# Kernel optimization log

Measured on AMD Instinct MI355X. Metric: run time of the kernel, lower is better.

The kernel has to match this reference:

```python
import jax, jax.numpy as jnp
import numpy as np

B, CATT, D, H, W = 4, 8, 48, 128, 256
CF, EMB, HEADS, WIN = 80, 64, 4, 3
WIN2 = WIN * WIN
HEAD_DIM = EMB // HEADS
SCALE = HEAD_DIM ** -0.5


def setup_inputs() -> dict:
    key = jax.random.key(0)
    ks = jax.random.split(key, 7)
    attn_vol = jax.random.normal(ks[0], (B, CATT, D, H, W), dtype=jnp.float32)
    feat_map = jax.random.normal(ks[1], (B, CF, H, W), dtype=jnp.float32)
    # disp_gap in [0,4) so roughly half the pixels satisfy (disp_gap >= 2)
    disp_gap = jax.random.uniform(ks[2], (B, 1, H, W), dtype=jnp.float32) * 4.0
    xav = (6.0 / (EMB + CF)) ** 0.5
    Wq = jax.random.uniform(ks[3], (EMB, CF), jnp.float32, -xav, xav)
    Wk = jax.random.uniform(ks[4], (EMB, CF), jnp.float32, -xav, xav)
    Wv = jax.random.uniform(ks[5], (EMB, CF), jnp.float32, -xav, xav)
    # out_proj weight is zero-initialized in the module; use small random for a
    # non-degenerate correctness baseline
    Wo = jax.random.normal(ks[6], (CATT, EMB), dtype=jnp.float32) * 0.02
    return {"attn_vol": attn_vol, "feat_map": feat_map, "disp_gap": disp_gap,
            "Wq": Wq, "Wk": Wk, "Wv": Wv, "Wo": Wo}


def _unfold3x3_torch_layout(x):
    # x: (B, E, H, W) -> (B, N, WIN2, E) matching torch's
    # unfold(...).transpose(1,2).view(B, N, win2, emb), where unfold channel
    # index is c*9 + w (channel-major). The subsequent view therefore MIXES
    # channels and window positions; we reproduce that exactly.
    b, e, h, w = x.shape
    p = WIN // 2
    xp = jnp.pad(x, ((0, 0), (0, 0), (p, p), (p, p)))
    pat = jnp.stack([xp[:, :, i:i + h, j:j + w]
                     for i in range(WIN) for j in range(WIN)], axis=2)  # (B,E,9,H,W)
    pat = pat.reshape(b, e * WIN2, h * w)          # torch unfold layout c*9+w
    pat = pat.transpose(0, 2, 1)                   # (B, N, E*9)
    return pat.reshape(b, h * w, WIN2, e)          # faithful (mixed) view


def reference(attn_vol, feat_map, disp_gap, Wq, Wk, Wv, Wo):
    b, c_att, d, h, w = attn_vol.shape
    n = h * w
    Q = jnp.einsum('bchw,ec->behw', feat_map, Wq)
    K = jnp.einsum('bchw,ec->behw', feat_map, Wk)
    V = jnp.einsum('bchw,ec->behw', feat_map, Wv)

    Ku = _unfold3x3_torch_layout(K)  # (B, N, 9, EMB)
    Vu = _unfold3x3_torch_layout(V)

    # split heads
    Qh = Q.reshape(b, EMB, n).transpose(0, 2, 1)
    Qh = Qh.reshape(b, n, HEADS, HEAD_DIM).transpose(0, 2, 1, 3)          # (B,h,N,hd)
    Kh = Ku.reshape(b, n, WIN2, HEADS, HEAD_DIM).transpose(0, 3, 1, 2, 4)  # (B,h,N,9,hd)
    Vh = Vu.reshape(b, n, WIN2, HEADS, HEAD_DIM).transpose(0, 3, 1, 2, 4)

    scores = jnp.einsum('bhnd,bhnwd->bhnw', Qh, Kh) * SCALE
    probs = jax.nn.softmax(scores, axis=-1)
    ctx = jnp.einsum('bhnw,bhnwd->bhnd', probs, Vh)                        # (B,h,N,hd)

    ctx = ctx.transpose(0, 2, 1, 3).reshape(b, n, EMB)
    delta2d = ctx.transpose(0, 2, 1).reshape(b, EMB, h, w)
    delta2d = jnp.einsum('behw,ae->bahw', delta2d, Wo)                     # (B,CATT,H,W)

    mask = (disp_gap >= 2.0).reshape(b, 1, 1, h, w)
    delta = jnp.where(mask, 0.0, delta2d[:, :, None, :, :])               # (B,CATT,D,H,W)
    return attn_vol + delta
```

## Files before the change

kernel.cpp:

```cpp
#include <hip/hip_runtime.h>
#include <math.h>

namespace {
constexpr int Bc   = 4;
constexpr int CATT = 8;
constexpr int Hh   = 128;
constexpr int Ww   = 256;
constexpr int CF   = 80;
constexpr int EMB  = 64;
constexpr int Nn   = Hh * Ww;
constexpr float SCALE = 0.25f;

constexpr int ROWP  = 264;
constexpr int PLANE = 130 * ROWP;
constexpr size_t WS_KVQ   = 0;
constexpr size_t WS_DELTA = (size_t)Bc * 192 * PLANE;
constexpr size_t WS_WT    = WS_DELTA + (size_t)Bc * CATT * Nn;
constexpr size_t WS_WOT   = WS_WT + (size_t)CF * 192;
constexpr size_t WS_END   = WS_WOT + 512;
constexpr size_t NEED_BYTES = WS_END * 4;

constexpr size_t OWS_KV    = 0;
constexpr size_t OWS_DELTA = (size_t)Bc * Nn * 128;
constexpr size_t OWS_WTKV  = OWS_DELTA + (size_t)Bc * CATT * Nn;
constexpr size_t OWS_WTQ   = OWS_WTKV + (size_t)CF * 128;
}


__global__ void prep_new_k(const float* __restrict__ Wq,
                           const float* __restrict__ Wk,
                           const float* __restrict__ Wv,
                           const float* __restrict__ Wo,
                           float* __restrict__ wt,
                           float* __restrict__ wot,
                           float* __restrict__ kvq) {
  const int t = blockIdx.x * blockDim.x + threadIdx.x;
  const int stride = gridDim.x * blockDim.x;
  for (int i = t; i < CF * 192; i += stride) {
    const int c = i / 192, o = i % 192;
    float v;
    if (o < 64)       v = Wq[o * CF + c] * SCALE;
    else if (o < 128) v = Wk[(o - 64) * CF + c];
    else              v = Wv[(o - 128) * CF + c];
    wt[i] = v;
  }
  for (int i = t; i < 512; i += stride) {
    const int e = i >> 3, a = i & 7;
    wot[i] = Wo[a * EMB + e];
  }
  const int HALO = 1552;
  for (int i = t; i < Bc * 192 * HALO; i += stride) {
    const int plane = i / HALO;
    const int r = i % HALO;
    int row, col;
    if (r < 264)        { row = 0;   col = r; }
    else if (r < 528)   { row = 129; col = r - 264; }
    else {
      const int rr = r - 528;
      row = (rr >> 3) + 1;
      const int c8 = rr & 7;
      col = (c8 < 4) ? c8 : (260 + c8 - 4);
    }
    kvq[(size_t)plane * PLANE + row * ROWP + col] = 0.f;
  }
}

__global__ __launch_bounds__(256) void qkv_new_k(const float* __restrict__ feat,
                                                 const float* __restrict__ wt,
                                                 float* __restrict__ kvq) {
  __shared__ float lf[CF][64];
  const int b  = blockIdx.y;
  const int n0 = blockIdx.x * 64;
  const int t  = threadIdx.x;

  const float* fb = feat + (size_t)b * CF * Nn + n0;
  for (int i = t; i < CF * 64; i += 256) {
    const int c = i >> 6, p = i & 63;
    lf[c][p] = fb[(size_t)c * Nn + p];
  }
  __syncthreads();

  const int og = t >> 4;
  const int p4 = (t & 15) * 4;

  float acc[12][4];
#pragma unroll
  for (int o = 0; o < 12; ++o)
#pragma unroll
    for (int j = 0; j < 4; ++j) acc[o][j] = 0.f;

  for (int c = 0; c < CF; ++c) {
    const float4 fv = *(const float4*)&lf[c][p4];
    const float fa[4] = {fv.x, fv.y, fv.z, fv.w};
    const float4 w0 = *(const float4*)&wt[c * 192 + og * 12];
    const float4 w1 = *(const float4*)&wt[c * 192 + og * 12 + 4];
    const float4 w2 = *(const float4*)&wt[c * 192 + og * 12 + 8];
    const float wv12[12] = {w0.x, w0.y, w0.z, w0.w, w1.x, w1.y, w1.z, w1.w,
                            w2.x, w2.y, w2.z, w2.w};
#pragma unroll
    for (int o = 0; o < 12; ++o)
#pragma unroll
      for (int j = 0; j < 4; ++j) acc[o][j] = fmaf(wv12[o], fa[j], acc[o][j]);
  }

  const int h = n0 >> 8, w0c = n0 & 255;
  float* bbase = kvq + (size_t)b * 192 * PLANE;
  const int rowoff = (h + 1) * ROWP + (w0c + 4) + p4;
#pragma unroll
  for (int o = 0; o < 12; ++o) {
    const int oo = og * 12 + o;
    *(float4*)&bbase[(size_t)oo * PLANE + rowoff] =
        make_float4(acc[o][0], acc[o][1], acc[o][2], acc[o][3]);
  }
}

template <int HD>
__device__ __forceinline__ void attn_core(const float* __restrict__ kb, int coff,
                                          const float* __restrict__ lwot,
                                          float* __restrict__ part) {
  float q16[16];
#pragma unroll
  for (int i = 0; i < 16; ++i)
    q16[i] = kb[(size_t)(HD * 16 + i) * PLANE + coff];

  float sc[9];
#pragma unroll
  for (int w2 = 0; w2 < 9; ++w2) {
    float s = 0.f;
#pragma unroll
    for (int i = 0; i < 16; ++i) {
      const int f = w2 * 64 + HD * 16 + i;
      const int e = f / 9, widx = f % 9;
      const int D = (widx / 3 - 1) * ROWP + (widx % 3 - 1);
      s = fmaf(q16[i], kb[(size_t)(64 + e) * PLANE + coff + D], s);
    }
    sc[w2] = s;
  }

  float m = sc[0];
#pragma unroll
  for (int w2 = 1; w2 < 9; ++w2) m = fmaxf(m, sc[w2]);
  float probs[9], ssum = 0.f;
#pragma unroll
  for (int w2 = 0; w2 < 9; ++w2) {
    probs[w2] = __expf(sc[w2] - m);
    ssum += probs[w2];
  }
  const float inv = 1.f / ssum;
#pragma unroll
  for (int w2 = 0; w2 < 9; ++w2) probs[w2] *= inv;

  float ctx[16];
#pragma unroll
  for (int i = 0; i < 16; ++i) {
    float c = 0.f;
#pragma unroll
    for (int w2 = 0; w2 < 9; ++w2) {
      const int f = w2 * 64 + HD * 16 + i;
      const int e = f / 9, widx = f % 9;
      const int D = (widx / 3 - 1) * ROWP + (widx % 3 - 1);
      c = fmaf(probs[w2], kb[(size_t)(128 + e) * PLANE + coff + D], c);
    }
    ctx[i] = c;
  }

#pragma unroll
  for (int a = 0; a < 8; ++a) {
    float p = 0.f;
#pragma unroll
    for (int i = 0; i < 16; ++i)
      p = fmaf(lwot[(HD * 16 + i) * 8 + a], ctx[i], p);
    part[a] = p;
  }
}

__global__ __launch_bounds__(256) void attn_new_k(const float* __restrict__ kvq,
                                                  const float* __restrict__ wot,
                                                  const float* __restrict__ disp,
                                                  float* __restrict__ delta) {
  __shared__ float lwot[512];
  __shared__ float lpart[4 * 576];
  const int b = blockIdx.y;
  const int t = threadIdx.x;
  for (int i = t; i < 512; i += 256) lwot[i] = wot[i];
  __syncthreads();

  const int hd = t >> 6, lane = t & 63;
  const int n = blockIdx.x * 64 + lane;
  const int h = n >> 8, w = n & 255;
  const int coff = (h + 1) * ROWP + (w + 4);
  const float* kb = kvq + (size_t)b * 192 * PLANE;

  float part[8];
  switch (hd) {
    case 0: attn_core<0>(kb, coff, lwot, part); break;
    case 1: attn_core<1>(kb, coff, lwot, part); break;
    case 2: attn_core<2>(kb, coff, lwot, part); break;
    default: attn_core<3>(kb, coff, lwot, part); break;
  }
#pragma unroll
  for (int a = 0; a < 8; ++a) lpart[hd * 576 + lane * 9 + a] = part[a];
  __syncthreads();

  const int px = t & 63, ag = t >> 6;
  const int nn = blockIdx.x * 64 + px;
  const bool zero = disp[(size_t)b * Nn + nn] >= 2.0f;
  float* dout = delta + (size_t)b * CATT * Nn + nn;
#pragma unroll
  for (int k = 0; k < 2; ++k) {
    const int a = ag * 2 + k;
    const float s = lpart[0 * 576 + px * 9 + a] + lpart[1 * 576 + px * 9 + a] +
                    lpart[2 * 576 + px * 9 + a] + lpart[3 * 576 + px * 9 + a];
    dout[(size_t)a * Nn] = zero ? 0.f : s;
  }
}

__global__ void prep_weights_k(const float* __restrict__ Wq,
                               const float* __restrict__ Wk,
                               const float* __restrict__ Wv,
                               float* __restrict__ wtkv,
                               float* __restrict__ wtq) {
  const int t = blockIdx.x * blockDim.x + threadIdx.x;
  const int stride = gridDim.x * blockDim.x;
  for (int i = t; i < CF * 128; i += stride) {
    const int c = i >> 7, o = i & 127;
    wtkv[i] = (o < 64) ? Wk[o * CF + c] : Wv[(o - 64) * CF + c];
  }
  for (int i = t; i < CF * 64; i += stride) {
    const int c = i >> 6, e = i & 63;
    wtq[i] = Wq[e * CF + c] * SCALE;
  }
}

__global__ __launch_bounds__(256) void qkv_k(const float* __restrict__ feat,
                                             const float* __restrict__ wtkv,
                                             float* __restrict__ kv) {
  __shared__ float lf[CF][64];
  const int b  = blockIdx.y;
  const int n0 = blockIdx.x * 64;
  const int t  = threadIdx.x;
  const float* fb = feat + (size_t)b * CF * Nn + n0;
  for (int i = t; i < CF * 64; i += 256) {
    const int c = i >> 6, p = i & 63;
    lf[c][p] = fb[(size_t)c * Nn + p];
  }
  __syncthreads();
  const int og = t >> 4;
  const int p4 = (t & 15) * 4;
  float acc[8][4];
#pragma unroll
  for (int o = 0; o < 8; ++o)
#pragma unroll
    for (int j = 0; j < 4; ++j) acc[o][j] = 0.f;
  for (int c = 0; c < CF; ++c) {
    const float4 fv = *(const float4*)&lf[c][p4];
    const float fa[4] = {fv.x, fv.y, fv.z, fv.w};
    const float4 wa = *(const float4*)&wtkv[c * 128 + og * 8];
    const float4 wb = *(const float4*)&wtkv[c * 128 + og * 8 + 4];
    const float wv8[8] = {wa.x, wa.y, wa.z, wa.w, wb.x, wb.y, wb.z, wb.w};
#pragma unroll
    for (int o = 0; o < 8; ++o)
#pragma unroll
      for (int j = 0; j < 4; ++j) acc[o][j] = fmaf(wv8[o], fa[j], acc[o][j]);
  }
  float* outb = kv + ((size_t)b * Nn + n0) * 128;
#pragma unroll
  for (int j = 0; j < 4; ++j) {
    const int p = p4 + j;
    *(float4*)&outb[(size_t)p * 128 + og * 8] =
        make_float4(acc[0][j], acc[1][j], acc[2][j], acc[3][j]);
    *(float4*)&outb[(size_t)p * 128 + og * 8 + 4] =
        make_float4(acc[4][j], acc[5][j], acc[6][j], acc[7][j]);
  }
}

__global__ __launch_bounds__(256) void attn_k(const float* __restrict__ feat,
                                              const float* __restrict__ kvbuf,
                                              const float* __restrict__ wtq,
                                              const float* __restrict__ Wo,
                                              const float* __restrict__ disp,
                                              float* __restrict__ delta) {
  const int b = blockIdx.y;
  const int n = blockIdx.x * 256 + threadIdx.x;
  const int h = n >> 8;
  const int w = n & 255;
  float q[EMB];
#pragma unroll
  for (int e = 0; e < EMB; ++e) q[e] = 0.f;
  {
    const float* fb = feat + (size_t)b * CF * Nn + n;
    for (int c = 0; c < CF; ++c) {
      const float fv = fb[(size_t)c * Nn];
#pragma unroll
      for (int e = 0; e < EMB; ++e) q[e] = fmaf(wtq[c * EMB + e], fv, q[e]);
    }
  }
  const float* kvb = kvbuf + (size_t)b * Nn * 128;
  float sc[36];
#pragma unroll
  for (int i = 0; i < 36; ++i) sc[i] = 0.f;
#pragma unroll
  for (int widx = 0; widx < 9; ++widx) {
    const int di = widx / 3 - 1, dj = widx % 3 - 1;
    const int hh = h + di, ww = w + dj;
    if (hh < 0 || hh >= Hh || ww < 0 || ww >= Ww) continue;
    const float4* kn = (const float4*)(kvb + (size_t)(hh * Ww + ww) * 128);
#pragma unroll
    for (int e4 = 0; e4 < 16; ++e4) {
      const float4 kk = kn[e4];
      const float ka[4] = {kk.x, kk.y, kk.z, kk.w};
#pragma unroll
      for (int j = 0; j < 4; ++j) {
        const int f = (e4 * 4 + j) * 9 + widx;
        const int w2 = f >> 6, e2 = f & 63;
        sc[(e2 >> 4) * 9 + w2] = fmaf(q[e2], ka[j], sc[(e2 >> 4) * 9 + w2]);
      }
    }
  }
  float probs[36];
#pragma unroll
  for (int hdx = 0; hdx < 4; ++hdx) {
    float m = sc[hdx * 9];
#pragma unroll
    for (int w2 = 1; w2 < 9; ++w2) m = fmaxf(m, sc[hdx * 9 + w2]);
    float s = 0.f;
#pragma unroll
    for (int w2 = 0; w2 < 9; ++w2) {
      const float ev = __expf(sc[hdx * 9 + w2] - m);
      probs[hdx * 9 + w2] = ev;
      s += ev;
    }
    const float inv = 1.f / s;
#pragma unroll
    for (int w2 = 0; w2 < 9; ++w2) probs[hdx * 9 + w2] *= inv;
  }
  float ctx[EMB];
#pragma unroll
  for (int e = 0; e < EMB; ++e) ctx[e] = 0.f;
#pragma unroll
  for (int widx = 0; widx < 9; ++widx) {
    const int di = widx / 3 - 1, dj = widx % 3 - 1;
    const int hh = h + di, ww = w + dj;
    if (hh < 0 || hh >= Hh || ww < 0 || ww >= Ww) continue;
    const float4* vn = (const float4*)(kvb + (size_t)(hh * Ww + ww) * 128 + 64);
#pragma unroll
    for (int e4 = 0; e4 < 16; ++e4) {
      const float4 vv = vn[e4];
      const float va[4] = {vv.x, vv.y, vv.z, vv.w};
#pragma unroll
      for (int j = 0; j < 4; ++j) {
        const int f = (e4 * 4 + j) * 9 + widx;
        const int w2 = f >> 6, e2 = f & 63;
        ctx[e2] = fmaf(probs[(e2 >> 4) * 9 + w2], va[j], ctx[e2]);
      }
    }
  }
  const bool zero = (disp[(size_t)b * Nn + n] >= 2.0f);
  float* dout = delta + (size_t)b * CATT * Nn + n;
#pragma unroll
  for (int a = 0; a < CATT; ++a) {
    float s = 0.f;
#pragma unroll
    for (int e = 0; e < EMB; ++e) s = fmaf(Wo[a * EMB + e], ctx[e], s);
    dout[(size_t)a * Nn] = zero ? 0.f : s;
  }
}

__global__ __launch_bounds__(256) void add_k(const float* __restrict__ av,
                                             const float* __restrict__ delta,
                                             float* __restrict__ out) {
  const unsigned i4 = blockIdx.x * 256u + threadIdx.x;
  const unsigned n4 = i4 & 8191u;
  const unsigned t2 = i4 >> 13;
  const unsigned bc = t2 / 48u;
  const float4 a  = ((const float4*)av)[i4];
  const float4 dl = ((const float4*)delta)[(size_t)bc * 8192u + n4];
  ((float4*)out)[i4] = make_float4(a.x + dl.x, a.y + dl.y, a.z + dl.z, a.w + dl.w);
}

extern "C" void kernel_launch(void* const* d_in, const int* in_sizes, int n_in,
                              void* d_out, int out_size, void* d_ws, size_t ws_size,
                              hipStream_t stream) {
  const float* attn_vol = (const float*)d_in[0];
  const float* feat     = (const float*)d_in[1];
  const float* disp     = (const float*)d_in[2];
  const float* Wq       = (const float*)d_in[3];
  const float* Wk       = (const float*)d_in[4];
  const float* Wv       = (const float*)d_in[5];
  const float* Wo       = (const float*)d_in[6];
  float* out            = (float*)d_out;
  float* ws             = (float*)d_ws;
  const int nf4 = out_size / 4;

  if (ws_size >= NEED_BYTES) {
    float* kvq   = ws + WS_KVQ;
    float* delta = ws + WS_DELTA;
    float* wt    = ws + WS_WT;
    float* wot   = ws + WS_WOT;
    hipLaunchKernelGGL(prep_new_k, dim3(512), dim3(256), 0, stream,
                       Wq, Wk, Wv, Wo, wt, wot, kvq);
    hipLaunchKernelGGL(qkv_new_k, dim3(Nn / 64, Bc), dim3(256), 0, stream,
                       feat, wt, kvq);
    hipLaunchKernelGGL(attn_new_k, dim3(Nn / 64, Bc), dim3(256), 0, stream,
                       kvq, wot, disp, delta);
    hipLaunchKernelGGL(add_k, dim3(nf4 / 256), dim3(256), 0, stream,
                       attn_vol, delta, out);
  } else {
    float* kv    = ws + OWS_KV;
    float* delta = ws + OWS_DELTA;
    float* wtkv  = ws + OWS_WTKV;
    float* wtq   = ws + OWS_WTQ;
    hipLaunchKernelGGL(prep_weights_k, dim3(40), dim3(256), 0, stream,
                       Wq, Wk, Wv, wtkv, wtq);
    hipLaunchKernelGGL(qkv_k, dim3(Nn / 64, Bc), dim3(256), 0, stream,
                       feat, wtkv, kv);
    hipLaunchKernelGGL(attn_k, dim3(Nn / 256, Bc), dim3(256), 0, stream,
                       feat, kv, wtq, Wo, disp, delta);
    hipLaunchKernelGGL(add_k, dim3(nf4 / 256), dim3(256), 0, stream,
                       attn_vol, delta, out);
  }
}
```

Measured before the change: 490.3 us.

## Fuse delta broadcast-add into attention kernel and vectorize halo zeroing for K/V

The attention kernel now adds its masked per-pixel delta directly to attn_vol across all 48 depth slices and writes the output, using nontemporal loads and stores. This removes the separate add kernel and the intermediate delta buffer round trip. Halo zeroing is changed to float4 stores and now covers only the K/V planes (channels 64..191), skipping the Q planes, which are only read at the centre. The fused kernel does the full 200MB stream from a grid shaped for the attention work, so memory-level parallelism may drop compared with the dedicated add kernel.

```diff
diff --git a/kernel.cpp b/kernel.cpp
--- a/kernel.cpp
+++ b/kernel.cpp
@@ -4,6 +4,7 @@
 namespace {
 constexpr int Bc   = 4;
 constexpr int CATT = 8;
+constexpr int Dd   = 48;
 constexpr int Hh   = 128;
 constexpr int Ww   = 256;
 constexpr int CF   = 80;
@@ -14,8 +15,7 @@
 constexpr int ROWP  = 264;
 constexpr int PLANE = 130 * ROWP;
 constexpr size_t WS_KVQ   = 0;
-constexpr size_t WS_DELTA = (size_t)Bc * 192 * PLANE;
-constexpr size_t WS_WT    = WS_DELTA + (size_t)Bc * CATT * Nn;
+constexpr size_t WS_WT    = (size_t)Bc * 192 * PLANE;
 constexpr size_t WS_WOT   = WS_WT + (size_t)CF * 192;
 constexpr size_t WS_END   = WS_WOT + 512;
 constexpr size_t NEED_BYTES = WS_END * 4;
@@ -48,20 +48,21 @@
     const int e = i >> 3, a = i & 7;
     wot[i] = Wo[a * EMB + e];
   }
-  const int HALO = 1552;
-  for (int i = t; i < Bc * 192 * HALO; i += stride) {
-    const int plane = i / HALO;
-    const int r = i % HALO;
-    int row, col;
-    if (r < 264)        { row = 0;   col = r; }
-    else if (r < 528)   { row = 129; col = r - 264; }
+  constexpr int HF4 = 388;
+  const float4 z4 = make_float4(0.f, 0.f, 0.f, 0.f);
+  for (int i = t; i < Bc * 128 * HF4; i += stride) {
+    const int f4 = i % HF4;
+    const int pl = i / HF4;
+    const size_t base = ((size_t)(pl / 128) * 192 + 64 + (pl % 128)) * PLANE;
+    int row, col4;
+    if (f4 < 66)        { row = 0;   col4 = f4 * 4; }
+    else if (f4 < 132)  { row = 129; col4 = (f4 - 66) * 4; }
     else {
-      const int rr = r - 528;
-      row = (rr >> 3) + 1;
-      const int c8 = rr & 7;
-      col = (c8 < 4) ? c8 : (260 + c8 - 4);
-    }
-    kvq[(size_t)plane * PLANE + row * ROWP + col] = 0.f;
+      const int rr = f4 - 132;
+      row = (rr >> 1) + 1;
+      col4 = (rr & 1) ? 260 : 0;
+    }
+    *(float4*)&kvq[base + (size_t)row * ROWP + col4] = z4;
   }
 }
 
@@ -174,10 +175,11 @@
   }
 }
 
-__global__ __launch_bounds__(256) void attn_new_k(const float* __restrict__ kvq,
-                                                  const float* __restrict__ wot,
-                                                  const float* __restrict__ disp,
-                                                  float* __restrict__ delta) {
+__global__ __launch_bounds__(256) void attn_fused_k(const float* __restrict__ kvq,
+                                                    const float* __restrict__ wot,
+                                                    const float* __restrict__ disp,
+                                                    const float* __restrict__ av,
+                                                    float* __restrict__ out) {
   __shared__ float lwot[512];
   __shared__ float lpart[4 * 576];
   const int b = blockIdx.y;
@@ -205,13 +207,31 @@
   const int px = t & 63, ag = t >> 6;
   const int nn = blockIdx.x * 64 + px;
   const bool zero = disp[(size_t)b * Nn + nn] >= 2.0f;
-  float* dout = delta + (size_t)b * CATT * Nn + nn;
+
+  float sv[2];
 #pragma unroll
   for (int k = 0; k < 2; ++k) {
     const int a = ag * 2 + k;
     const float s = lpart[0 * 576 + px * 9 + a] + lpart[1 * 576 + px * 9 + a] +
                     lpart[2 * 576 + px * 9 + a] + lpart[3 * 576 + px * 9 + a];
-    dout[(size_t)a * Nn] = zero ? 0.f : s;
+    sv[k] = zero ? 0.f : s;
+  }
+
+#pragma unroll
+  for (int k = 0; k < 2; ++k) {
+    const int a = ag * 2 + k;
+    const size_t pb = ((size_t)(b * CATT + a) * Dd) * Nn + nn;
+    const float* ab = av + pb;
+    float* ob = out + pb;
+    for (int d0 = 0; d0 < Dd; d0 += 8) {
+      float tb[8];
+#pragma unroll
+      for (int j = 0; j < 8; ++j)
+        tb[j] = __builtin_nontemporal_load(ab + (size_t)(d0 + j) * Nn);
+#pragma unroll
+      for (int j = 0; j < 8; ++j)
+        __builtin_nontemporal_store(tb[j] + sv[k], ob + (size_t)(d0 + j) * Nn);
+    }
   }
 }
 
@@ -393,18 +413,15 @@
   const int nf4 = out_size / 4;
 
   if (ws_size >= NEED_BYTES) {
-    float* kvq   = ws + WS_KVQ;
-    float* delta = ws + WS_DELTA;
-    float* wt    = ws + WS_WT;
-    float* wot   = ws + WS_WOT;
+    float* kvq = ws + WS_KVQ;
+    float* wt  = ws + WS_WT;
+    float* wot = ws + WS_WOT;
     hipLaunchKernelGGL(prep_new_k, dim3(512), dim3(256), 0, stream,
                        Wq, Wk, Wv, Wo, wt, wot, kvq);
     hipLaunchKernelGGL(qkv_new_k, dim3(Nn / 64, Bc), dim3(256), 0, stream,
                        feat, wt, kvq);
-    hipLaunchKernelGGL(attn_new_k, dim3(Nn / 64, Bc), dim3(256), 0, stream,
-                       kvq, wot, disp, delta);
-    hipLaunchKernelGGL(add_k, dim3(nf4 / 256), dim3(256), 0, stream,
-                       attn_vol, delta, out);
+    hipLaunchKernelGGL(attn_fused_k, dim3(Nn / 64, Bc), dim3(256), 0, stream,
+                       kvq, wot, disp, attn_vol, out);
   } else {
     float* kv    = ws + OWS_KV;
     float* delta = ws + OWS_DELTA;
```

Measured after the change: 484.7 us. Within noise of the previous version (-1.1%).
